# Kernel tuning notes

Hardware: AMD Instinct MI355X
Metric: run time of the kernel (lower is better)

## Reference

```python
import jax, jax.numpy as jnp
import numpy as np

S, B, E, H, AW = 4096, 2, 768, 12, 512  # seq, batch, embed, heads, attention_window


def _longformer_local_attn(query, Wq, bq, Wk, bk, Wv, bv):
    # query: [S, B, E] (seq-first, as in the torch module); returns [S, B, E]
    S_, B_, E_ = query.shape
    H_ = H
    D = E_ // H_
    W = AW // 2  # one-sided window (HF Longformer uses window//2 each side)
    x = query.transpose(1, 0, 2)  # [B, S, E]

    q = (x @ Wq + bq).reshape(B_, S_, H_, D) * (1.0 / jnp.sqrt(jnp.asarray(D, x.dtype)))
    k = (x @ Wk + bk).reshape(B_, S_, H_, D)
    v = (x @ Wv + bv).reshape(B_, S_, H_, D)

    nc = S_ // W  # number of query chunks of size W
    # pad keys/values by W on each side so every chunk sees a 3W key window
    kp = jnp.pad(k, ((0, 0), (W, W), (0, 0), (0, 0)))
    vp = jnp.pad(v, ((0, 0), (W, W), (0, 0), (0, 0)))
    # padded-coordinate indices of the 3W key window for each chunk: [nc, 3W]
    idx = jnp.arange(nc)[:, None] * W + jnp.arange(3 * W)[None, :]
    kc = kp[:, idx]  # [B, nc, 3W, H, D]
    vc = vp[:, idx]  # [B, nc, 3W, H, D]
    qc = q.reshape(B_, nc, W, H_, D)

    # banded scores: [B, H, nc, W, 3W]
    scores = jnp.einsum('bcqhd,bckhd->bhcqk', qc, kc)

    # mask: within-band (|rel| <= W) and inside the real sequence
    rel = (jnp.arange(3 * W) - W)[None, :] - jnp.arange(W)[:, None]  # [W, 3W]
    band = jnp.abs(rel) <= W
    abs_k = idx - W  # absolute key index, [nc, 3W]
    in_seq = (abs_k >= 0) & (abs_k < S_)
    mask = band[None, :, :] & in_seq[:, None, :]  # [nc, W, 3W]

    scores = jnp.where(mask[None, None], scores, -jnp.inf)
    attn = jax.nn.softmax(scores, axis=-1)
    out = jnp.einsum('bhcqk,bckhd->bcqhd', attn, vc).reshape(B_, S_, E_)
    return out.transpose(1, 0, 2)  # back to [S, B, E]


def setup_inputs() -> dict:
    key = jax.random.key(0)
    ks = jax.random.split(key, 4)
    scale = 0.02
    return {
        'query': jax.random.normal(ks[0], (S, B, E), jnp.float32),
        'Wq': jax.random.normal(ks[1], (E, E), jnp.float32) * scale,
        'bq': jnp.zeros((E,), jnp.float32),
        'Wk': jax.random.normal(ks[2], (E, E), jnp.float32) * scale,
        'bk': jnp.zeros((E,), jnp.float32),
        'Wv': jax.random.normal(ks[3], (E, E), jnp.float32) * scale,
        'bv': jnp.zeros((E,), jnp.float32),
    }


def reference(query, Wq, bq, Wk, bk, Wv, bv):
    # dropout is identity in eval mode; no global tokens (global mask defaults to zeros)
    return _longformer_local_attn(query, Wq, bq, Wk, bk, Wv, bv)
```

## Files before the change

kernel.cpp:

```cpp
#include <hip/hip_runtime.h>

#define S_ 4096
#define B_ 2
#define E_ 768
#define H_ 12
#define D_ 64

typedef __attribute__((ext_vector_type(8))) short short8;
typedef __attribute__((ext_vector_type(4))) float f32x4;
typedef unsigned short u16;
typedef unsigned int u32;

__device__ __forceinline__ u16 f2bf(float f) {
  union { float f; u32 u; } v; v.f = f;
  u32 r = v.u + 0x7FFFu + ((v.u >> 16) & 1u);
  return (u16)(r >> 16);
}

__device__ __forceinline__ void gl_lds16(const void* g, void* l) {
  __builtin_amdgcn_global_load_lds((const __attribute__((address_space(1))) u32*)g,
                                   (__attribute__((address_space(3))) u32*)l, 16, 0, 0);
}

__global__ __launch_bounds__(192) void k_convert_x(const float* __restrict__ q,
                                                   u16* __restrict__ x) {
  int m = blockIdx.x;
  int e = threadIdx.x * 4;
  int b = m >> 12, s = m & 4095;
  const float4 v = *(const float4*)&q[((s << 1) + b) * 768 + e];
  ushort4 o;
  o.x = f2bf(v.x); o.y = f2bf(v.y); o.z = f2bf(v.z); o.w = f2bf(v.w);
  *(ushort4*)&x[m * 768 + e] = o;
}

__global__ __launch_bounds__(256) void k_transpose_w(const float* __restrict__ w0,
                                                     const float* __restrict__ w1,
                                                     const float* __restrict__ w2,
                                                     u16* __restrict__ wt) {
  __shared__ float tile[32][33];
  const float* w = blockIdx.z == 0 ? w0 : (blockIdx.z == 1 ? w1 : w2);
  int k0 = blockIdx.x * 32, n0 = blockIdx.y * 32;
  int tx = threadIdx.x & 31, ty = threadIdx.x >> 5;
#pragma unroll
  for (int i = 0; i < 4; i++)
    tile[ty + i * 8][tx] = w[(k0 + ty + i * 8) * 768 + n0 + tx];
  __syncthreads();
  u16* o = wt + blockIdx.z * 768 * 768;
#pragma unroll
  for (int i = 0; i < 4; i++)
    o[(n0 + ty + i * 8) * 768 + k0 + tx] = f2bf(tile[tx][ty + i * 8]);
}

__global__ __launch_bounds__(256, 2) void k_gemm_qkv(
    const u16* __restrict__ x, const u16* __restrict__ wt,
    const float* __restrict__ bq, const float* __restrict__ bk,
    const float* __restrict__ bv,
    u16* __restrict__ qb, u16* __restrict__ kb, u16* __restrict__ vt) {
  __shared__ __align__(16) u16 smem[24576];
  const int tid = threadIdx.x;
  const int lane = tid & 63, wave = tid >> 6;
  const int wm = wave >> 1, wn = wave & 1;
  const int l15 = lane & 15, lg = lane >> 4;

  const int bid = blockIdx.x;
  const int xcd = bid & 7, idx = bid >> 3;
  const int m0 = (xcd * 4 + idx / 18) * 256;
  const int n0g = (idx % 18) * 128;
  const int z = n0g / 768, j0 = n0g % 768;
  const u16* wz = wt + (size_t)z * 768 * 768;

  f32x4 acc[8][4] = {};

  auto stage = [&](int buf, int kt) {
#pragma unroll
    for (int c = 0; c < 4; c++) {
      int ci = c * 256 + tid;
      int row = ci >> 2, cp = ci & 3;
      int sc = cp ^ ((row >> 1) & 3);
      gl_lds16(&x[(size_t)(m0 + row) * 768 + kt + sc * 8],
               &smem[buf * 12288 + (c * 256 + wave * 64) * 8]);
    }
#pragma unroll
    for (int c = 0; c < 2; c++) {
      int ci = c * 256 + tid;
      int row = ci >> 2, cp = ci & 3;
      int sc = cp ^ ((row >> 1) & 3);
      gl_lds16(&wz[(size_t)(j0 + row) * 768 + kt + sc * 8],
               &smem[buf * 12288 + 8192 + (c * 256 + wave * 64) * 8]);
    }
  };

  stage(0, 0);
  __syncthreads();
  const int kc = lg ^ ((l15 >> 1) & 3);
  for (int t = 0; t < 24; t++) {
    const int buf = t & 1;
    if (t < 23) stage(buf ^ 1, (t + 1) * 32);
    short8 a[8], b[4];
#pragma unroll
    for (int mf = 0; mf < 8; mf++)
      a[mf] = *(const short8*)&smem[buf * 12288 +
                                    (wm * 128 + mf * 16 + l15) * 32 + kc * 8];
#pragma unroll
    for (int nf = 0; nf < 4; nf++)
      b[nf] = *(const short8*)&smem[buf * 12288 + 8192 +
                                    (wn * 64 + nf * 16 + l15) * 32 + kc * 8];
#pragma unroll
    for (int mf = 0; mf < 8; mf++)
#pragma unroll
      for (int nf = 0; nf < 4; nf++)
        acc[mf][nf] = __builtin_amdgcn_mfma_f32_16x16x32_bf16(a[mf], b[nf], acc[mf][nf], 0, 0, 0);
    __syncthreads();
  }

  u16* ep = &smem[wave * 4608];
  const float* bias_p = (z == 0) ? bq : (z == 1 ? bk : bv);
  const float sc_ = (z == 0) ? 0.125f : 1.0f;
  const int r8 = lane >> 3, cn = lane & 7;
  if (z < 2) {
    u16* t = (z == 0) ? qb : kb;
#pragma unroll
    for (int hh = 0; hh < 2; hh++) {
      __syncthreads();
#pragma unroll
      for (int mfl = 0; mfl < 4; mfl++) {
        int mf = hh * 4 + mfl;
#pragma unroll
        for (int nf = 0; nf < 4; nf++) {
          float bias = bias_p[j0 + wn * 64 + nf * 16 + l15];
#pragma unroll
          for (int r = 0; r < 4; r++)
            ep[(mfl * 16 + lg * 4 + r) * 72 + nf * 16 + l15] =
                f2bf((acc[mf][nf][r] + bias) * sc_);
        }
      }
      __syncthreads();
#pragma unroll
      for (int i = 0; i < 8; i++) {
        int rl = i * 8 + r8;
        short8 v = *(const short8*)&ep[rl * 72 + cn * 8];
        *(short8*)&t[(size_t)(m0 + wm * 128 + hh * 64 + rl) * 768 +
                     j0 + wn * 64 + cn * 8] = v;
      }
    }
  } else {
    const int bb = m0 >> 12, srow = m0 & 4095;
#pragma unroll
    for (int hh = 0; hh < 2; hh++) {
      __syncthreads();
#pragma unroll
      for (int nf = 0; nf < 4; nf++) {
        float bias = bias_p[j0 + wn * 64 + nf * 16 + l15];
#pragma unroll
        for (int mfl = 0; mfl < 4; mfl++) {
          int mf = hh * 4 + mfl;
          ushort4 pk;
          pk.x = f2bf(acc[mf][nf][0] + bias);
          pk.y = f2bf(acc[mf][nf][1] + bias);
          pk.z = f2bf(acc[mf][nf][2] + bias);
          pk.w = f2bf(acc[mf][nf][3] + bias);
          *(ushort4*)&ep[(nf * 16 + l15) * 72 + mfl * 16 + lg * 4] = pk;
        }
      }
      __syncthreads();
#pragma unroll
      for (int i = 0; i < 8; i++) {
        int nl = i * 8 + r8;
        int n = j0 + wn * 64 + nl;
        int h = n >> 6, d = n & 63;
        short8 v = *(const short8*)&ep[nl * 72 + cn * 8];
        *(short8*)&vt[(((size_t)(bb * 12 + h) * 64 + d) << 12) +
                      srow + wm * 128 + hh * 64 + cn * 8] = v;
      }
    }
  }
}

__global__ __launch_bounds__(256) void k_attn(const u16* __restrict__ qb,
                                              const u16* __restrict__ kb,
                                              const u16* __restrict__ vt,
                                              float* __restrict__ out) {
  __shared__ __align__(16) u16 Ks[2][64 * 64];
  __shared__ __align__(16) u16 Vs[2][64 * 64];
  __shared__ __align__(16) u16 pl[4][32 * 72];
  const int tid = threadIdx.x;
  const int lane = tid & 63, wave = tid >> 6;
  const int l15 = lane & 15, lg = lane >> 4;

  const int bid = blockIdx.x;
  const int xcd = bid & 7, i = bid >> 3;
  const int pair = xcd * 3 + (i >> 5);
  const int chunk = i & 31;
  const int b = pair / 12, h = pair % 12;
  const int s0 = chunk * 128;
  const int q0 = s0 + wave * 32;

  short8 qf[2][2];
#pragma unroll
  for (int mf = 0; mf < 2; mf++)
#pragma unroll
    for (int ks = 0; ks < 2; ks++)
      qf[mf][ks] = *(const short8*)&qb[(size_t)((b << 12) + q0 + mf * 16 + l15) * 768 +
                                       h * 64 + ks * 32 + lg * 8];

  f32x4 o[2][4] = {};
  float lsum[2][4] = {};

  int t0 = s0 - 256; if (t0 < 0) t0 = 0;
  int t1 = s0 + 320; if (t1 > 4032) t1 = 4032;

  auto stage = [&](int buf, int kb0) {
#pragma unroll
    for (int c = 0; c < 2; c++) {
      int ci = c * 256 + tid;
      int row = ci >> 3, cc = ci & 7;
      int sc = cc ^ (row & 7);
      gl_lds16(&kb[(size_t)((b << 12) + kb0 + row) * 768 + h * 64 + sc * 8],
               &Ks[buf][(c * 256 + wave * 64) * 8]);
      gl_lds16(&vt[((size_t)((b * 12 + h) * 64 + row) << 12) + kb0 + sc * 8],
               &Vs[buf][(c * 256 + wave * 64) * 8]);
    }
  };

  stage(0, t0);
  int buf = 0;
  for (int kb0 = t0; kb0 <= t1; kb0 += 64) {
    if (kb0 + 64 <= t1) stage(buf ^ 1, kb0 + 64);
    __syncthreads();
    const bool act = (kb0 + 63 >= q0 - 256) && (kb0 <= q0 + 31 + 256);
    if (act) {
      f32x4 sf[2][4] = {};
#pragma unroll
      for (int ks = 0; ks < 2; ks++) {
        short8 bkf[4];
#pragma unroll
        for (int nf = 0; nf < 4; nf++) {
          int row = nf * 16 + l15;
          bkf[nf] = *(const short8*)&Ks[buf][row * 64 + (((ks * 4 + lg) ^ (row & 7)) * 8)];
        }
#pragma unroll
        for (int mf = 0; mf < 2; mf++)
#pragma unroll
          for (int nf = 0; nf < 4; nf++)
            sf[mf][nf] = __builtin_amdgcn_mfma_f32_16x16x32_bf16(qf[mf][ks], bkf[nf], sf[mf][nf], 0, 0, 0);
      }
      if (kb0 < q0 - 192 || kb0 > q0 + 192) {
#pragma unroll
        for (int mf = 0; mf < 2; mf++)
#pragma unroll
          for (int nf = 0; nf < 4; nf++) {
            int kj = kb0 + nf * 16 + l15;
#pragma unroll
            for (int r = 0; r < 4; r++) {
              int qi = q0 + mf * 16 + lg * 4 + r;
              if ((unsigned)(kj - qi + 256) > 512u) sf[mf][nf][r] = -3e38f;
            }
          }
      }
      u16* plw = pl[wave];
#pragma unroll
      for (int mf = 0; mf < 2; mf++)
#pragma unroll
        for (int nf = 0; nf < 4; nf++)
#pragma unroll
          for (int r = 0; r < 4; r++) {
            float p = __expf(sf[mf][nf][r]);
            lsum[mf][r] += p;
            plw[(mf * 16 + lg * 4 + r) * 72 + nf * 16 + l15] = f2bf(p);
          }
      short8 pa[2][2];
#pragma unroll
      for (int mf = 0; mf < 2; mf++)
#pragma unroll
        for (int ks = 0; ks < 2; ks++)
          pa[mf][ks] = *(const short8*)&plw[(mf * 16 + l15) * 72 + ks * 32 + lg * 8];
#pragma unroll
      for (int ks = 0; ks < 2; ks++) {
        short8 bvf[4];
#pragma unroll
        for (int df = 0; df < 4; df++) {
          int row = df * 16 + l15;
          bvf[df] = *(const short8*)&Vs[buf][row * 64 + (((ks * 4 + lg) ^ (row & 7)) * 8)];
        }
#pragma unroll
        for (int mf = 0; mf < 2; mf++)
#pragma unroll
          for (int df = 0; df < 4; df++)
            o[mf][df] = __builtin_amdgcn_mfma_f32_16x16x32_bf16(pa[mf][ks], bvf[df], o[mf][df], 0, 0, 0);
      }
    }
    __syncthreads();
    buf ^= 1;
  }

#pragma unroll
  for (int mf = 0; mf < 2; mf++)
#pragma unroll
    for (int r = 0; r < 4; r++) {
      float l = lsum[mf][r];
      l += __shfl_xor(l, 1); l += __shfl_xor(l, 2);
      l += __shfl_xor(l, 4); l += __shfl_xor(l, 8);
      lsum[mf][r] = l;
    }

#pragma unroll
  for (int mf = 0; mf < 2; mf++)
#pragma unroll
    for (int df = 0; df < 4; df++)
#pragma unroll
      for (int r = 0; r < 4; r++) {
        int s = q0 + mf * 16 + lg * 4 + r;
        out[(size_t)(s * 2 + b) * 768 + h * 64 + df * 16 + l15] =
            o[mf][df][r] / lsum[mf][r];
      }
}

extern "C" void kernel_launch(void* const* d_in, const int* in_sizes, int n_in,
                              void* d_out, int out_size, void* d_ws, size_t ws_size,
                              hipStream_t stream) {
  const float* query = (const float*)d_in[0];
  const float* Wq = (const float*)d_in[1];
  const float* bq = (const float*)d_in[2];
  const float* Wk = (const float*)d_in[3];
  const float* bk = (const float*)d_in[4];
  const float* Wv = (const float*)d_in[5];
  const float* bv = (const float*)d_in[6];
  float* out = (float*)d_out;

  char* ws = (char*)d_ws;
  size_t off = 0;
  auto alloc = [&](size_t bytes) {
    void* p = ws + off;
    off = (off + bytes + 255) & ~(size_t)255;
    return p;
  };
  u16* x  = (u16*)alloc((size_t)8192 * 768 * 2);
  u16* wt = (u16*)alloc((size_t)3 * 768 * 768 * 2);
  u16* qb = (u16*)alloc((size_t)8192 * 768 * 2);
  u16* kb = (u16*)alloc((size_t)8192 * 768 * 2);
  u16* vt = (u16*)alloc((size_t)8192 * 768 * 2);

  hipLaunchKernelGGL(k_convert_x, dim3(8192), dim3(192), 0, stream, query, x);
  hipLaunchKernelGGL(k_transpose_w, dim3(24, 24, 3), dim3(256), 0, stream, Wq, Wk, Wv, wt);
  hipLaunchKernelGGL(k_gemm_qkv, dim3(576), dim3(256), 0, stream,
                     x, wt, bq, bk, bv, qb, kb, vt);
  hipLaunchKernelGGL(k_attn, dim3(768), dim3(256), 0, stream, qb, kb, vt, out);
}
```

Before: 170.1 us.

## Triple-buffer QKV GEMM loads with vmcnt waits and merge prep kernels

The QKV GEMM main loop moves from double buffering with two __syncthreads per iteration to a three-stage LDS ring. Loads are issued two k-steps ahead, and completion is tracked with explicit s_waitcnt vmcnt plus a single barrier, so more global-to-LDS latency is hidden. Shared memory per block grows from 48KB to 72KB, which may limit blocks per CU. Separately, the x conversion and weight transpose kernels are merged into one launch to save a kernel launch, at the cost of 64 idle threads in each conversion block.

```diff
diff --git a/kernel.cpp b/kernel.cpp
--- a/kernel.cpp
+++ b/kernel.cpp
@@ -22,33 +22,38 @@
                                    (__attribute__((address_space(3))) u32*)l, 16, 0, 0);
 }
 
-__global__ __launch_bounds__(192) void k_convert_x(const float* __restrict__ q,
-                                                   u16* __restrict__ x) {
-  int m = blockIdx.x;
-  int e = threadIdx.x * 4;
-  int b = m >> 12, s = m & 4095;
-  const float4 v = *(const float4*)&q[((s << 1) + b) * 768 + e];
-  ushort4 o;
-  o.x = f2bf(v.x); o.y = f2bf(v.y); o.z = f2bf(v.z); o.w = f2bf(v.w);
-  *(ushort4*)&x[m * 768 + e] = o;
-}
-
-__global__ __launch_bounds__(256) void k_transpose_w(const float* __restrict__ w0,
-                                                     const float* __restrict__ w1,
-                                                     const float* __restrict__ w2,
-                                                     u16* __restrict__ wt) {
+__global__ __launch_bounds__(256) void k_prep(const float* __restrict__ q,
+                                              const float* __restrict__ w0,
+                                              const float* __restrict__ w1,
+                                              const float* __restrict__ w2,
+                                              u16* __restrict__ x,
+                                              u16* __restrict__ wt) {
   __shared__ float tile[32][33];
-  const float* w = blockIdx.z == 0 ? w0 : (blockIdx.z == 1 ? w1 : w2);
-  int k0 = blockIdx.x * 32, n0 = blockIdx.y * 32;
-  int tx = threadIdx.x & 31, ty = threadIdx.x >> 5;
-#pragma unroll
-  for (int i = 0; i < 4; i++)
-    tile[ty + i * 8][tx] = w[(k0 + ty + i * 8) * 768 + n0 + tx];
-  __syncthreads();
-  u16* o = wt + blockIdx.z * 768 * 768;
-#pragma unroll
-  for (int i = 0; i < 4; i++)
-    o[(n0 + ty + i * 8) * 768 + k0 + tx] = f2bf(tile[tx][ty + i * 8]);
+  const int bid = blockIdx.x;
+  if (bid < 1728) {
+    const int z = bid / 576, r = bid % 576;
+    const int k0 = (r / 24) * 32, n0 = (r % 24) * 32;
+    const float* w = z == 0 ? w0 : (z == 1 ? w1 : w2);
+    const int tx = threadIdx.x & 31, ty = threadIdx.x >> 5;
+#pragma unroll
+    for (int i = 0; i < 4; i++)
+      tile[ty + i * 8][tx] = w[(k0 + ty + i * 8) * 768 + n0 + tx];
+    __syncthreads();
+    u16* o = wt + (size_t)z * 768 * 768;
+#pragma unroll
+    for (int i = 0; i < 4; i++)
+      o[(n0 + ty + i * 8) * 768 + k0 + tx] = f2bf(tile[tx][ty + i * 8]);
+  } else {
+    const int m = bid - 1728;
+    const int e = threadIdx.x * 4;
+    if (e < 768) {
+      const int b = m >> 12, s = m & 4095;
+      const float4 v = *(const float4*)&q[((s << 1) + b) * 768 + e];
+      ushort4 o;
+      o.x = f2bf(v.x); o.y = f2bf(v.y); o.z = f2bf(v.z); o.w = f2bf(v.w);
+      *(ushort4*)&x[m * 768 + e] = o;
+    }
+  }
 }
 
 __global__ __launch_bounds__(256, 2) void k_gemm_qkv(
@@ -56,7 +61,7 @@
     const float* __restrict__ bq, const float* __restrict__ bk,
     const float* __restrict__ bv,
     u16* __restrict__ qb, u16* __restrict__ kb, u16* __restrict__ vt) {
-  __shared__ __align__(16) u16 smem[24576];
+  __shared__ __align__(16) u16 smem[36864];
   const int tid = threadIdx.x;
   const int lane = tid & 63, wave = tid >> 6;
   const int wm = wave >> 1, wn = wave & 1;
@@ -91,26 +96,32 @@
   };
 
   stage(0, 0);
-  __syncthreads();
+  stage(1, 32);
   const int kc = lg ^ ((l15 >> 1) & 3);
+  int cur = 0;
   for (int t = 0; t < 24; t++) {
-    const int buf = t & 1;
-    if (t < 23) stage(buf ^ 1, (t + 1) * 32);
+    if (t < 23) { asm volatile("s_waitcnt vmcnt(6)" ::: "memory"); }
+    else       { asm volatile("s_waitcnt vmcnt(0)" ::: "memory"); }
+    __builtin_amdgcn_s_barrier();
+    __builtin_amdgcn_sched_barrier(0);
+    if (t < 22) {
+      int st = cur + 2; if (st >= 3) st -= 3;
+      stage(st, (t + 2) * 32);
+    }
+    const int base = cur * 12288;
     short8 a[8], b[4];
 #pragma unroll
     for (int mf = 0; mf < 8; mf++)
-      a[mf] = *(const short8*)&smem[buf * 12288 +
-                                    (wm * 128 + mf * 16 + l15) * 32 + kc * 8];
+      a[mf] = *(const short8*)&smem[base + (wm * 128 + mf * 16 + l15) * 32 + kc * 8];
 #pragma unroll
     for (int nf = 0; nf < 4; nf++)
-      b[nf] = *(const short8*)&smem[buf * 12288 + 8192 +
-                                    (wn * 64 + nf * 16 + l15) * 32 + kc * 8];
+      b[nf] = *(const short8*)&smem[base + 8192 + (wn * 64 + nf * 16 + l15) * 32 + kc * 8];
 #pragma unroll
     for (int mf = 0; mf < 8; mf++)
 #pragma unroll
       for (int nf = 0; nf < 4; nf++)
         acc[mf][nf] = __builtin_amdgcn_mfma_f32_16x16x32_bf16(a[mf], b[nf], acc[mf][nf], 0, 0, 0);
-    __syncthreads();
+    cur = (cur + 1 == 3) ? 0 : cur + 1;
   }
 
   u16* ep = &smem[wave * 4608];
@@ -340,8 +351,8 @@
   u16* kb = (u16*)alloc((size_t)8192 * 768 * 2);
   u16* vt = (u16*)alloc((size_t)8192 * 768 * 2);
 
-  hipLaunchKernelGGL(k_convert_x, dim3(8192), dim3(192), 0, stream, query, x);
-  hipLaunchKernelGGL(k_transpose_w, dim3(24, 24, 3), dim3(256), 0, stream, Wq, Wk, Wv, wt);
+  hipLaunchKernelGGL(k_prep, dim3(1728 + 8192), dim3(256), 0, stream,
+                     query, Wq, Wk, Wv, x, wt);
   hipLaunchKernelGGL(k_gemm_qkv, dim3(576), dim3(256), 0, stream,
                      x, wt, bq, bk, bv, qb, kb, vt);
   hipLaunchKernelGGL(k_attn, dim3(768), dim3(256), 0, stream, qb, kb, vt, out);
```

New measurement: 166.4 us. 1.02x faster.
